# Optimization experiments

Measured on AMD Instinct MI355X. Metric: run time of the kernel, lower is better.

Reference implementation:

```python
import jax, jax.numpy as jnp
import numpy as np

B, S, D, H = 2, 2048, 1024, 16
DK = D // H


def setup_inputs() -> dict:
    key = jax.random.key(0)
    ks = jax.random.split(key, 11)
    s = 1.0 / np.sqrt(D)
    return {
        "q": jax.random.normal(ks[0], (B, S, D), jnp.float32),
        "k": jax.random.normal(ks[1], (B, S, D), jnp.float32),
        "v": jax.random.normal(ks[2], (B, S, D), jnp.float32),
        "mask": jnp.ones((B, 1, S, S), jnp.int32),
        "Wq": jax.random.normal(ks[3], (D, D), jnp.float32) * s,
        "bq": jnp.zeros((D,), jnp.float32),
        "Wk": jax.random.normal(ks[4], (D, D), jnp.float32) * s,
        "bk": jnp.zeros((D,), jnp.float32),
        "Wv": jax.random.normal(ks[5], (D, D), jnp.float32) * s,
        "bv": jnp.zeros((D,), jnp.float32),
        "Wo": jax.random.normal(ks[6], (D, D), jnp.float32) * s,
        "bo": jnp.zeros((D,), jnp.float32),
    }


def reference(q, k, v, mask, Wq, bq, Wk, bk, Wv, bv, Wo, bo):
    # Note: original torch code calls non-in-place masked_fill and discards the
    # result, so the mask has no mathematical effect; we preserve that.
    qh = (q @ Wq + bq).reshape(B, S, H, DK).transpose(0, 2, 1, 3)  # [B,H,S,DK]
    kh = (k @ Wk + bk).reshape(B, S, H, DK).transpose(0, 2, 1, 3)
    vh = (v @ Wv + bv).reshape(B, S, H, DK).transpose(0, 2, 1, 3)
    scores = jnp.einsum("bhqd,bhkd->bhqk", qh, kh) / jnp.sqrt(jnp.float32(DK))
    attn = jax.nn.softmax(scores, axis=-1)
    out = jnp.einsum("bhqk,bhkd->bhqd", attn, vh)  # [B,H,S,DK]
    out = out.transpose(0, 2, 1, 3).reshape(B, S, D)
    return out @ Wo + bo
```

## Files before the change

### kernel.cpp

```cpp
#include <hip/hip_runtime.h>

#define S_LEN    2048
#define D_MODEL  1024
#define N_HEADS  16
#define HEAD_DIM 64
#define BATCH    2

typedef __bf16 bf16x8 __attribute__((ext_vector_type(8)));
typedef float  floatx4 __attribute__((ext_vector_type(4)));

__device__ __forceinline__ unsigned short f2bf(float f) {
    union { float f; unsigned int u; } v;
    v.f = f;
    unsigned int u = v.u;
    u += 0x7fffu + ((u >> 16) & 1u);
    return (unsigned short)(u >> 16);
}

__device__ __forceinline__ unsigned int pk_rne(float a, float b) {
    union { float f; unsigned int u; } ua, ub;
    ua.f = a; ub.f = b;
    unsigned int x = ua.u + 0x7fffu + ((ua.u >> 16) & 1u);
    unsigned int y = ub.u + 0x7fffu + ((ub.u >> 16) & 1u);
    return __builtin_amdgcn_perm(y, x, 0x07060302);
}

__device__ __forceinline__ void gload_lds16(const unsigned short* g, unsigned short* l) {
    __builtin_amdgcn_global_load_lds(
        (const __attribute__((address_space(1))) void*)(const void*)g,
        (__attribute__((address_space(3))) void*)(void*)l,
        16, 0, 0);
}

struct PrepArgs {
    const float* src[3]; unsigned short* dst[3];
    const float* W[4];   unsigned short* Wt[4];
};

#define CONV_BLOCKS (3 * 4096)

__global__ void prep_kernel(PrepArgs args) {
    const int bid = blockIdx.x;
    if (bid < CONV_BLOCKS) {
        const int t   = bid >> 12;
        const int blk = bid & 4095;
        const int i   = blk * 256 + threadIdx.x;
        float4 f = reinterpret_cast<const float4*>(args.src[t])[i];
        ushort4 o;
        o.x = f2bf(f.x); o.y = f2bf(f.y); o.z = f2bf(f.z); o.w = f2bf(f.w);
        reinterpret_cast<ushort4*>(args.dst[t])[i] = o;
    } else {
        __shared__ unsigned short tile[64][65];
        const int r  = bid - CONV_BLOCKS;
        const int w  = r >> 8;
        const int xy = r & 255;
        const int n0 = (xy & 15) * 64, k0 = (xy >> 4) * 64;
        const float* W = args.W[w];
        unsigned short* Wt = args.Wt[w];
        for (int rep = 0; rep < 16; ++rep) {
            int e = rep * 256 + threadIdx.x;
            int kk = e >> 6, nn = e & 63;
            tile[kk][nn] = f2bf(W[(size_t)(k0 + kk) * D_MODEL + n0 + nn]);
        }
        __syncthreads();
        for (int rep = 0; rep < 16; ++rep) {
            int e = rep * 256 + threadIdx.x;
            int nn = e >> 6, kk = e & 63;
            Wt[(size_t)(n0 + nn) * D_MODEL + k0 + kk] = tile[kk][nn];
        }
    }
}

template <int TM, int TN, int MODE>
__device__ __forceinline__
void gemm_body(const unsigned short* __restrict__ A,
               const unsigned short* __restrict__ Bt,
               const float* __restrict__ bias,
               void* __restrict__ out,
               int m0, int n0, float scale,
               unsigned short* As, unsigned short* Bs) {
    constexpr int MT = TM / 32;
    constexpr int NT = TN / 32;
    const int tid  = threadIdx.x;
    const int wid  = tid >> 6;
    const int lane = tid & 63;

    floatx4 acc[MT][NT];
#pragma unroll
    for (int i = 0; i < MT; ++i)
#pragma unroll
        for (int j = 0; j < NT; ++j) acc[i][j] = (floatx4)0.0f;

    const int srow = lane >> 2;
    const int gch  = (lane & 3) ^ ((srow >> 1) & 3);
    const int wr = (wid >> 1) * (TM / 2);
    const int wc = (wid & 1) * (TN / 2);
    const int fr = lane & 15;
    const int fq = lane >> 4;
    const int swz = (fq ^ ((fr >> 1) & 3)) * 8;

    for (int k0 = 0; k0 < D_MODEL; k0 += 32) {
        if (k0) __syncthreads();
#pragma unroll
        for (int ci = 0; ci < (TM + TN) / 64; ++ci) {
            const int c = wid + ci * 4;
            if (c < TM / 16) {
                const int row = c * 16 + srow;
                gload_lds16(A + (size_t)(m0 + row) * D_MODEL + k0 + gch * 8, As + c * 512);
            } else {
                const int cb = c - TM / 16;
                const int row = cb * 16 + srow;
                gload_lds16(Bt + (size_t)(n0 + row) * D_MODEL + k0 + gch * 8, Bs + cb * 512);
            }
        }
        __syncthreads();

        bf16x8 af[MT], bfv[NT];
#pragma unroll
        for (int t = 0; t < MT; ++t)
            af[t] = *reinterpret_cast<const bf16x8*>(As + (wr + t * 16 + fr) * 32 + swz);
#pragma unroll
        for (int t = 0; t < NT; ++t)
            bfv[t] = *reinterpret_cast<const bf16x8*>(Bs + (wc + t * 16 + fr) * 32 + swz);
#pragma unroll
        for (int mt = 0; mt < MT; ++mt)
#pragma unroll
            for (int nt = 0; nt < NT; ++nt)
                acc[mt][nt] = __builtin_amdgcn_mfma_f32_16x16x32_bf16(af[mt], bfv[nt], acc[mt][nt], 0, 0, 0);
    }

#pragma unroll
    for (int nt = 0; nt < NT; ++nt) {
        const int n = n0 + wc + nt * 16 + fr;
        const float bval = bias[n];
#pragma unroll
        for (int mt = 0; mt < MT; ++mt) {
#pragma unroll
            for (int r = 0; r < 4; ++r) {
                const int m = m0 + wr + mt * 16 + fq * 4 + r;
                const float val = (acc[mt][nt][r] + bval) * scale;
                if (MODE == 2) {
                    reinterpret_cast<float*>(out)[(size_t)m * D_MODEL + n] = val;
                } else {
                    const int b = m >> 11, s = m & (S_LEN - 1);
                    const int h = n >> 6, dk = n & 63;
                    const unsigned short o16 = f2bf(val);
                    if (MODE == 0)
                        reinterpret_cast<unsigned short*>(out)[(((size_t)(b * N_HEADS + h)) * S_LEN + s) * HEAD_DIM + dk] = o16;
                    else
                        reinterpret_cast<unsigned short*>(out)[(((size_t)(b * N_HEADS + h)) * HEAD_DIM + dk) * S_LEN + s] = o16;
                }
            }
        }
    }
}

struct QKVArgs {
    const unsigned short* A[3];
    const unsigned short* Bt[3];
    const float* bias[3];
    unsigned short* out[3];
};

__global__ __launch_bounds__(256)
void qkv_gemm_kernel(QKVArgs args) {
    __shared__ __align__(16) unsigned short As[128 * 32];
    __shared__ __align__(16) unsigned short Bs[128 * 32];
    const int z = blockIdx.z;
    const int m0 = blockIdx.y * 128;
    const int n0 = blockIdx.x * 128;
    if (z == 0)
        gemm_body<128, 128, 0>(args.A[0], args.Bt[0], args.bias[0], args.out[0], m0, n0, 0.18033688011112f, As, Bs);
    else if (z == 1)
        gemm_body<128, 128, 0>(args.A[1], args.Bt[1], args.bias[1], args.out[1], m0, n0, 1.0f, As, Bs);
    else
        gemm_body<128, 128, 1>(args.A[2], args.Bt[2], args.bias[2], args.out[2], m0, n0, 1.0f, As, Bs);
}

__global__ __launch_bounds__(256)
void oproj_gemm_kernel(const unsigned short* __restrict__ A,
                       const unsigned short* __restrict__ Bt,
                       const float* __restrict__ bias,
                       float* __restrict__ out) {
    __shared__ __align__(16) unsigned short As[64 * 32];
    __shared__ __align__(16) unsigned short Bs[128 * 32];
    gemm_body<64, 128, 2>(A, Bt, bias, out, blockIdx.y * 64, blockIdx.x * 128, 1.0f, As, Bs);
}

__global__ __launch_bounds__(256)
void attn_kernel(const unsigned short* __restrict__ qhp,
                 const unsigned short* __restrict__ khp,
                 const unsigned short* __restrict__ vtp,
                 unsigned short* __restrict__ outp) {
    __shared__ __align__(16) unsigned short Qs[64 * 64];
    __shared__ __align__(16) unsigned short Ks[64 * 64];
    __shared__ __align__(16) unsigned short Vs[64 * 64];
    __shared__ __align__(16) unsigned short Ps[4][16 * 72];

    const int tid  = threadIdx.x;
    const int wid  = tid >> 6;
    const int lane = tid & 63;
    const int b = blockIdx.z, h = blockIdx.y;
    const int q0 = blockIdx.x * 64;

    const unsigned short* qbase = qhp + (size_t)(b * N_HEADS + h) * S_LEN * HEAD_DIM;
    const unsigned short* kbase = khp + (size_t)(b * N_HEADS + h) * S_LEN * HEAD_DIM;
    const unsigned short* vbase = vtp + (size_t)(b * N_HEADS + h) * HEAD_DIM * S_LEN;

    const int srow = lane >> 3;
    const int gch  = (lane & 7) ^ srow;
    const int fr = lane & 15;
    const int fq = lane >> 4;
    const int sw7 = fr & 7;

#pragma unroll
    for (int i = 0; i < 2; ++i) {
        const int c = wid * 2 + i;
        const int row = c * 8 + srow;
        gload_lds16(qbase + (size_t)(q0 + row) * HEAD_DIM + gch * 8, Qs + c * 512);
    }
    __syncthreads();

    bf16x8 qf[2];
#pragma unroll
    for (int kk = 0; kk < 2; ++kk)
        qf[kk] = *reinterpret_cast<const bf16x8*>(
            Qs + (wid * 16 + fr) * 64 + (((kk * 4 + fq) ^ sw7) * 8));

    floatx4 o_acc[4];
#pragma unroll
    for (int j = 0; j < 4; ++j) o_acc[j] = (floatx4)0.0f;
    float l_sum = 0.0f;

    for (int kv0 = 0; kv0 < S_LEN; kv0 += 64) {
        if (kv0) __syncthreads();
#pragma unroll
        for (int i = 0; i < 2; ++i) {
            const int c = wid * 2 + i;
            const int row = c * 8 + srow;
            gload_lds16(kbase + (size_t)(kv0 + row) * HEAD_DIM + gch * 8, Ks + c * 512);
            gload_lds16(vbase + (size_t)row * S_LEN + kv0 + gch * 8,       Vs + c * 512);
        }
        __syncthreads();

        floatx4 st[4];
#pragma unroll
        for (int j = 0; j < 4; ++j) st[j] = (floatx4)0.0f;
#pragma unroll
        for (int nt = 0; nt < 4; ++nt) {
#pragma unroll
            for (int kk = 0; kk < 2; ++kk) {
                bf16x8 kf = *reinterpret_cast<const bf16x8*>(
                    Ks + (nt * 16 + fr) * 64 + (((kk * 4 + fq) ^ sw7) * 8));
                st[nt] = __builtin_amdgcn_mfma_f32_16x16x32_bf16(kf, qf[kk], st[nt], 0, 0, 0);
            }
        }

#pragma unroll
        for (int nt = 0; nt < 4; ++nt) {
            float p0 = __builtin_amdgcn_exp2f(st[nt][0]);
            float p1 = __builtin_amdgcn_exp2f(st[nt][1]);
            float p2 = __builtin_amdgcn_exp2f(st[nt][2]);
            float p3 = __builtin_amdgcn_exp2f(st[nt][3]);
            l_sum += (p0 + p1) + (p2 + p3);
            uint2 w;
            w.x = pk_rne(p0, p1);
            w.y = pk_rne(p2, p3);
            *reinterpret_cast<uint2*>(Ps[wid] + fr * 72 + nt * 16 + fq * 4) = w;
        }
        __asm__ volatile("s_waitcnt lgkmcnt(0)" ::: "memory");

#pragma unroll
        for (int kk = 0; kk < 2; ++kk) {
            bf16x8 pf = *reinterpret_cast<const bf16x8*>(Ps[wid] + fr * 72 + kk * 32 + fq * 8);
#pragma unroll
            for (int dt = 0; dt < 4; ++dt) {
                bf16x8 vf = *reinterpret_cast<const bf16x8*>(
                    Vs + (dt * 16 + fr) * 64 + (((kk * 4 + fq) ^ sw7) * 8));
                o_acc[dt] = __builtin_amdgcn_mfma_f32_16x16x32_bf16(pf, vf, o_acc[dt], 0, 0, 0);
            }
        }
    }

    float l = l_sum;
    l += __shfl_xor(l, 16);
    l += __shfl_xor(l, 32);
    float linv[4];
#pragma unroll
    for (int r = 0; r < 4; ++r)
        linv[r] = __builtin_amdgcn_rcpf(__shfl(l, fq * 4 + r));
#pragma unroll
    for (int dt = 0; dt < 4; ++dt) {
#pragma unroll
        for (int r = 0; r < 4; ++r) {
            const int s  = q0 + wid * 16 + fq * 4 + r;
            const int dk = dt * 16 + fr;
            const float val = o_acc[dt][r] * linv[r];
            outp[((size_t)(b * S_LEN + s)) * D_MODEL + h * HEAD_DIM + dk] = f2bf(val);
        }
    }
}

extern "C" void kernel_launch(void* const* d_in, const int* in_sizes, int n_in,
                              void* d_out, int out_size, void* d_ws, size_t ws_size,
                              hipStream_t stream) {
    (void)in_sizes; (void)n_in; (void)out_size; (void)ws_size;
    const float* q  = (const float*)d_in[0];
    const float* k  = (const float*)d_in[1];
    const float* v  = (const float*)d_in[2];
    const float* Wq = (const float*)d_in[4];
    const float* bq = (const float*)d_in[5];
    const float* Wk = (const float*)d_in[6];
    const float* bk = (const float*)d_in[7];
    const float* Wv = (const float*)d_in[8];
    const float* bv = (const float*)d_in[9];
    const float* Wo = (const float*)d_in[10];
    const float* bo = (const float*)d_in[11];
    float* out = (float*)d_out;

    char* ws = (char*)d_ws;
    const size_t SZ_ACT = (size_t)BATCH * S_LEN * D_MODEL * 2;
    const size_t SZ_W   = (size_t)D_MODEL * D_MODEL * 2;
    unsigned short* qb   = (unsigned short*)(ws);
    unsigned short* kb   = (unsigned short*)(ws + SZ_ACT);
    unsigned short* vb   = (unsigned short*)(ws + 2 * SZ_ACT);
    unsigned short* Wqt  = (unsigned short*)(ws + 3 * SZ_ACT);
    unsigned short* Wkt  = (unsigned short*)(ws + 3 * SZ_ACT + SZ_W);
    unsigned short* Wvt  = (unsigned short*)(ws + 3 * SZ_ACT + 2 * SZ_W);
    unsigned short* Wot  = (unsigned short*)(ws + 3 * SZ_ACT + 3 * SZ_W);
    unsigned short* qhb  = (unsigned short*)(ws + 3 * SZ_ACT + 4 * SZ_W);
    unsigned short* khb  = (unsigned short*)(ws + 4 * SZ_ACT + 4 * SZ_W);
    unsigned short* vtb  = (unsigned short*)(ws + 5 * SZ_ACT + 4 * SZ_W);
    unsigned short* attn = qb;

    PrepArgs pargs;
    pargs.src[0] = q;  pargs.src[1] = k;  pargs.src[2] = v;
    pargs.dst[0] = qb; pargs.dst[1] = kb; pargs.dst[2] = vb;
    pargs.W[0] = Wq;  pargs.W[1] = Wk;  pargs.W[2] = Wv;  pargs.W[3] = Wo;
    pargs.Wt[0] = Wqt; pargs.Wt[1] = Wkt; pargs.Wt[2] = Wvt; pargs.Wt[3] = Wot;
    prep_kernel<<<dim3(CONV_BLOCKS + 1024), 256, 0, stream>>>(pargs);

    QKVArgs gargs;
    gargs.A[0] = qb;  gargs.A[1] = kb;  gargs.A[2] = vb;
    gargs.Bt[0] = Wqt; gargs.Bt[1] = Wkt; gargs.Bt[2] = Wvt;
    gargs.bias[0] = bq; gargs.bias[1] = bk; gargs.bias[2] = bv;
    gargs.out[0] = qhb; gargs.out[1] = khb; gargs.out[2] = vtb;
    qkv_gemm_kernel<<<dim3(8, 32, 3), 256, 0, stream>>>(gargs);

    attn_kernel<<<dim3(S_LEN / 64, N_HEADS, BATCH), 256, 0, stream>>>(qhb, khb, vtb, attn);

    oproj_gemm_kernel<<<dim3(8, 64), 256, 0, stream>>>(attn, Wot, bo, out);
}
```

Before: 264.3 us.

## Switch attention to 32x32x16 MFMA with in-register P via permlane32 swap

Rewrites the attention kernel to use 2 waves of 128 threads, each owning 32 query rows, with 32x32x16 bf16 MFMA instructions in place of 16x16x32. The softmax probabilities are repacked into the A-operand layout with permlane32_swap in registers, which removes the per-wave LDS P buffer and its wait. Each block now issues fewer waves over the same K/V tiles, trading occupancy and latency hiding for fewer LDS round-trips and larger MFMA tiles. The exp is still taken without max subtraction, as before.

```diff
diff --git a/kernel.cpp b/kernel.cpp
--- a/kernel.cpp
+++ b/kernel.cpp
@@ -8,6 +8,8 @@
 
 typedef __bf16 bf16x8 __attribute__((ext_vector_type(8)));
 typedef float  floatx4 __attribute__((ext_vector_type(4)));
+typedef float  floatx16 __attribute__((ext_vector_type(16)));
+typedef int    intx2   __attribute__((ext_vector_type(2)));
 
 __device__ __forceinline__ unsigned short f2bf(float f) {
     union { float f; unsigned int u; } v;
@@ -187,7 +189,7 @@
     gemm_body<64, 128, 2>(A, Bt, bias, out, blockIdx.y * 64, blockIdx.x * 128, 1.0f, As, Bs);
 }
 
-__global__ __launch_bounds__(256)
+__global__ __launch_bounds__(128)
 void attn_kernel(const unsigned short* __restrict__ qhp,
                  const unsigned short* __restrict__ khp,
                  const unsigned short* __restrict__ vtp,
@@ -195,10 +197,9 @@
     __shared__ __align__(16) unsigned short Qs[64 * 64];
     __shared__ __align__(16) unsigned short Ks[64 * 64];
     __shared__ __align__(16) unsigned short Vs[64 * 64];
-    __shared__ __align__(16) unsigned short Ps[4][16 * 72];
 
     const int tid  = threadIdx.x;
-    const int wid  = tid >> 6;
+    const int ww   = tid >> 6;
     const int lane = tid & 63;
     const int b = blockIdx.z, h = blockIdx.y;
     const int q0 = blockIdx.x * 64;
@@ -207,96 +208,107 @@
     const unsigned short* kbase = khp + (size_t)(b * N_HEADS + h) * S_LEN * HEAD_DIM;
     const unsigned short* vbase = vtp + (size_t)(b * N_HEADS + h) * HEAD_DIM * S_LEN;
 
+    const int c31 = lane & 31;
+    const int hh  = lane >> 5;
+    const int l7  = lane & 7;
     const int srow = lane >> 3;
     const int gch  = (lane & 7) ^ srow;
-    const int fr = lane & 15;
-    const int fq = lane >> 4;
-    const int sw7 = fr & 7;
-
-#pragma unroll
-    for (int i = 0; i < 2; ++i) {
-        const int c = wid * 2 + i;
+
+#pragma unroll
+    for (int i = 0; i < 4; ++i) {
+        const int c = ww * 4 + i;
         const int row = c * 8 + srow;
         gload_lds16(qbase + (size_t)(q0 + row) * HEAD_DIM + gch * 8, Qs + c * 512);
     }
     __syncthreads();
 
-    bf16x8 qf[2];
-#pragma unroll
-    for (int kk = 0; kk < 2; ++kk)
-        qf[kk] = *reinterpret_cast<const bf16x8*>(
-            Qs + (wid * 16 + fr) * 64 + (((kk * 4 + fq) ^ sw7) * 8));
-
-    floatx4 o_acc[4];
-#pragma unroll
-    for (int j = 0; j < 4; ++j) o_acc[j] = (floatx4)0.0f;
+    bf16x8 qf[4];
+#pragma unroll
+    for (int ks = 0; ks < 4; ++ks)
+        qf[ks] = *reinterpret_cast<const bf16x8*>(
+            Qs + (ww * 32 + c31) * 64 + (((2 * ks + hh) ^ l7) * 8));
+
+    floatx16 o_acc[2];
+#pragma unroll
+    for (int i = 0; i < 2; ++i) o_acc[i] = (floatx16)0.0f;
     float l_sum = 0.0f;
 
     for (int kv0 = 0; kv0 < S_LEN; kv0 += 64) {
         if (kv0) __syncthreads();
 #pragma unroll
-        for (int i = 0; i < 2; ++i) {
-            const int c = wid * 2 + i;
+        for (int i = 0; i < 4; ++i) {
+            const int c = ww * 4 + i;
             const int row = c * 8 + srow;
             gload_lds16(kbase + (size_t)(kv0 + row) * HEAD_DIM + gch * 8, Ks + c * 512);
             gload_lds16(vbase + (size_t)row * S_LEN + kv0 + gch * 8,       Vs + c * 512);
         }
         __syncthreads();
 
-        floatx4 st[4];
-#pragma unroll
-        for (int j = 0; j < 4; ++j) st[j] = (floatx4)0.0f;
-#pragma unroll
-        for (int nt = 0; nt < 4; ++nt) {
-#pragma unroll
-            for (int kk = 0; kk < 2; ++kk) {
+        floatx16 st[2];
+#pragma unroll
+        for (int i = 0; i < 2; ++i) st[i] = (floatx16)0.0f;
+#pragma unroll
+        for (int ks = 0; ks < 4; ++ks) {
+#pragma unroll
+            for (int sub = 0; sub < 2; ++sub) {
                 bf16x8 kf = *reinterpret_cast<const bf16x8*>(
-                    Ks + (nt * 16 + fr) * 64 + (((kk * 4 + fq) ^ sw7) * 8));
-                st[nt] = __builtin_amdgcn_mfma_f32_16x16x32_bf16(kf, qf[kk], st[nt], 0, 0, 0);
-            }
-        }
-
-#pragma unroll
-        for (int nt = 0; nt < 4; ++nt) {
-            float p0 = __builtin_amdgcn_exp2f(st[nt][0]);
-            float p1 = __builtin_amdgcn_exp2f(st[nt][1]);
-            float p2 = __builtin_amdgcn_exp2f(st[nt][2]);
-            float p3 = __builtin_amdgcn_exp2f(st[nt][3]);
-            l_sum += (p0 + p1) + (p2 + p3);
-            uint2 w;
-            w.x = pk_rne(p0, p1);
-            w.y = pk_rne(p2, p3);
-            *reinterpret_cast<uint2*>(Ps[wid] + fr * 72 + nt * 16 + fq * 4) = w;
-        }
-        __asm__ volatile("s_waitcnt lgkmcnt(0)" ::: "memory");
-
-#pragma unroll
-        for (int kk = 0; kk < 2; ++kk) {
-            bf16x8 pf = *reinterpret_cast<const bf16x8*>(Ps[wid] + fr * 72 + kk * 32 + fq * 8);
-#pragma unroll
-            for (int dt = 0; dt < 4; ++dt) {
+                    Ks + (sub * 32 + c31) * 64 + (((2 * ks + hh) ^ l7) * 8));
+                st[sub] = __builtin_amdgcn_mfma_f32_32x32x16_bf16(kf, qf[ks], st[sub], 0, 0, 0);
+            }
+        }
+
+        float p[32];
+#pragma unroll
+        for (int sub = 0; sub < 2; ++sub) {
+#pragma unroll
+            for (int r = 0; r < 16; r += 4) {
+                float e0 = __builtin_amdgcn_exp2f(st[sub][r + 0]);
+                float e1 = __builtin_amdgcn_exp2f(st[sub][r + 1]);
+                float e2 = __builtin_amdgcn_exp2f(st[sub][r + 2]);
+                float e3 = __builtin_amdgcn_exp2f(st[sub][r + 3]);
+                l_sum += (e0 + e1) + (e2 + e3);
+                p[sub * 16 + r + 0] = e0; p[sub * 16 + r + 1] = e1;
+                p[sub * 16 + r + 2] = e2; p[sub * 16 + r + 3] = e3;
+            }
+        }
+
+        bf16x8 paf[4];
+#pragma unroll
+        for (int j = 0; j < 4; ++j) {
+            const int base = (j >> 1) * 16 + (j & 1) * 8;
+            unsigned int A0 = pk_rne(p[base + 0], p[base + 1]);
+            unsigned int A1 = pk_rne(p[base + 2], p[base + 3]);
+            unsigned int B0 = pk_rne(p[base + 4], p[base + 5]);
+            unsigned int B1 = pk_rne(p[base + 6], p[base + 7]);
+            intx2 s0 = __builtin_amdgcn_permlane32_swap((int)A0, (int)B0, false, false);
+            intx2 s1 = __builtin_amdgcn_permlane32_swap((int)A1, (int)B1, false, false);
+            union { int i[4]; bf16x8 v; } fb;
+            fb.i[0] = s0[0]; fb.i[1] = s1[0]; fb.i[2] = s0[1]; fb.i[3] = s1[1];
+            paf[j] = fb.v;
+        }
+
+#pragma unroll
+        for (int j = 0; j < 4; ++j) {
+#pragma unroll
+            for (int dsub = 0; dsub < 2; ++dsub) {
                 bf16x8 vf = *reinterpret_cast<const bf16x8*>(
-                    Vs + (dt * 16 + fr) * 64 + (((kk * 4 + fq) ^ sw7) * 8));
-                o_acc[dt] = __builtin_amdgcn_mfma_f32_16x16x32_bf16(pf, vf, o_acc[dt], 0, 0, 0);
-            }
-        }
-    }
-
-    float l = l_sum;
-    l += __shfl_xor(l, 16);
-    l += __shfl_xor(l, 32);
-    float linv[4];
-#pragma unroll
-    for (int r = 0; r < 4; ++r)
-        linv[r] = __builtin_amdgcn_rcpf(__shfl(l, fq * 4 + r));
-#pragma unroll
-    for (int dt = 0; dt < 4; ++dt) {
-#pragma unroll
-        for (int r = 0; r < 4; ++r) {
-            const int s  = q0 + wid * 16 + fq * 4 + r;
-            const int dk = dt * 16 + fr;
-            const float val = o_acc[dt][r] * linv[r];
-            outp[((size_t)(b * S_LEN + s)) * D_MODEL + h * HEAD_DIM + dk] = f2bf(val);
+                    Vs + (dsub * 32 + c31) * 64 + (((2 * j + hh) ^ l7) * 8));
+                o_acc[dsub] = __builtin_amdgcn_mfma_f32_32x32x16_bf16(paf[j], vf, o_acc[dsub], 0, 0, 0);
+            }
+        }
+    }
+
+    l_sum += __shfl_xor(l_sum, 32);
+#pragma unroll
+    for (int r = 0; r < 16; ++r) {
+        const int qr = (r & 3) + 8 * (r >> 2) + 4 * hh;
+        const float linv = __builtin_amdgcn_rcpf(__shfl(l_sum, qr));
+        const int s = q0 + ww * 32 + qr;
+#pragma unroll
+        for (int dsub = 0; dsub < 2; ++dsub) {
+            const int dk = dsub * 32 + c31;
+            outp[((size_t)(b * S_LEN + s)) * D_MODEL + h * HEAD_DIM + dk] =
+                f2bf(o_acc[dsub][r] * linv);
         }
     }
 }
@@ -347,7 +359,7 @@
     gargs.out[0] = qhb; gargs.out[1] = khb; gargs.out[2] = vtb;
     qkv_gemm_kernel<<<dim3(8, 32, 3), 256, 0, stream>>>(gargs);
 
-    attn_kernel<<<dim3(S_LEN / 64, N_HEADS, BATCH), 256, 0, stream>>>(qhb, khb, vtb, attn);
+    attn_kernel<<<dim3(S_LEN / 64, N_HEADS, BATCH), 128, 0, stream>>>(qhb, khb, vtb, attn);
 
     oproj_gemm_kernel<<<dim3(8, 64), 256, 0, stream>>>(attn, Wot, bo, out);
 }
```

Result: no change. 262.5 us (-0.7%).
